# Kernel optimization log

Measured on AMD Instinct MI355X. Metric: run time of the kernel, lower is better.

The kernel has to match this reference:

```python
import jax, jax.numpy as jnp
import numpy as np

S = 128          # spatial grid size per axis
N = 100000       # active voxels
C_IN = 32
C_OUT = 32
FS = 3           # filter size per axis -> 27 offsets


def _build_rulebook():
    """Build submanifold-conv rulebook: for each active site and each of the
    27 filter offsets, the index of the active neighbor (or masked out)."""
    rng = np.random.default_rng(0)
    coords = rng.integers(0, S, size=(2 * N, 3))
    lin = coords[:, 0] * S * S + coords[:, 1] * S + coords[:, 2]
    lin = np.unique(lin)[:N]                      # sorted unique active sites
    xyz = np.stack([lin // (S * S), (lin // S) % S, lin % S], axis=1)  # [N,3]
    offs = np.stack(np.meshgrid(*([np.arange(FS) - FS // 2] * 3), indexing='ij'), -1).reshape(-1, 3)  # [27,3]
    nb = xyz[:, None, :] + offs[None, :, :]       # [N,27,3]
    inb = np.all((nb >= 0) & (nb < S), axis=-1)   # in-bounds
    nb_lin = nb[..., 0] * S * S + nb[..., 1] * S + nb[..., 2]
    pos = np.searchsorted(lin, nb_lin)
    pos_c = np.clip(pos, 0, N - 1)
    found = inb & (lin[pos_c] == nb_lin)
    nbr_idx = np.where(found, pos_c, 0).astype(np.int32)   # [N,27]
    return nbr_idx, found


def setup_inputs() -> dict:
    key = jax.random.key(0)
    k1, k2 = jax.random.split(key)
    nbr_idx, nbr_mask = _build_rulebook()
    K = FS ** 3
    std = (2.0 / C_IN / K) ** 0.5   # matches module init
    return {
        'features': jax.random.normal(k1, (N, C_IN), dtype=jnp.float32),
        'weight': std * jax.random.normal(k2, (K, C_IN, C_OUT), dtype=jnp.float32),
        'bias': jnp.zeros((C_OUT,), dtype=jnp.float32),
        'nbr_idx': jnp.asarray(nbr_idx),
        'nbr_mask': jnp.asarray(nbr_mask),
    }


def reference(features, weight, bias, nbr_idx, nbr_mask):
    # Submanifold sparse conv: gather active neighbors per filter offset,
    # multiply by per-offset [Cin,Cout] weight, accumulate at active sites.
    gathered = jnp.where(nbr_mask[:, :, None], features[nbr_idx], 0.0)  # [N,K,Cin]
    out = jnp.einsum('nki,kio->no', gathered, weight) + bias            # [N,Cout]
    return out
```

## Files before the change

### kernel.cpp

```cpp
#include <hip/hip_runtime.h>
#include <hip/hip_bf16.h>

#define NVOX 100000
#define CIN 32
#define COUT 32
#define KOFF 27
#define KPAD 28

typedef __attribute__((ext_vector_type(8))) short short8;
typedef __attribute__((ext_vector_type(4))) float float4v;
typedef __attribute__((ext_vector_type(4))) int   int4v;

__device__ __forceinline__ short f2bf(float x) {
    union { float f; unsigned u; } v; v.f = x;
    unsigned u = v.u;
    u += 0x7FFFu + ((u >> 16) & 1u);
    return (short)(u >> 16);
}

__global__ __launch_bounds__(256) void feat_cvt_kernel(
    const float* __restrict__ feat, unsigned short* __restrict__ fbf)
{
    int i = (blockIdx.x * 256 + threadIdx.x) * 4;
    if (i < NVOX * CIN) {
        float4v f = *(const float4v*)(feat + i);
        short s[4] = { f2bf(f.x), f2bf(f.y), f2bf(f.z), f2bf(f.w) };
        *(ulonglong1*)(fbf + i) = *(ulonglong1*)s;
    } else if (i < (NVOX + 1) * CIN) {
        short s[4] = { 0, 0, 0, 0 };
        *(ulonglong1*)(fbf + i) = *(ulonglong1*)s;
    }
}

__global__ __launch_bounds__(256) void wgt_cvt_kernel(
    const float* __restrict__ weight, short8* __restrict__ wfrag)
{
    int g = blockIdx.x * 256 + threadIdx.x;
    if (g >= KOFF * 2 * 64) return;
    int k   = g >> 7;
    int rem = g & 127;
    int t   = rem >> 6;
    int ln  = rem & 63;
    int co  = t * 16 + (ln & 15);
    int cib = (ln >> 4) * 8;
    const float* wp = weight + (k * CIN + cib) * COUT + co;
    short8 b;
#pragma unroll
    for (int j = 0; j < 8; ++j) b[j] = f2bf(wp[j * COUT]);
    wfrag[g] = b;
}

__global__ __launch_bounds__(256) void enc_fold_kernel(
    const int* __restrict__ nbr_idx, const int* __restrict__ nbr_mask,
    int* __restrict__ encb)
{
    int v = blockIdx.x * 4 + (threadIdx.x >> 6);
    int k = threadIdx.x & 63;
    if (v >= NVOX || k >= KPAD) return;
    int e;
    if (k < KOFF) {
        int id = nbr_idx[v * KOFF + k];
        int mk = nbr_mask[v * KOFF + k];
        e = (mk ? id : NVOX) << 6;
    } else {
        e = NVOX << 6;
    }
    encb[v * KPAD + k] = e;
}

__global__ __launch_bounds__(512, 4) void subm_conv_kernel(
    const unsigned short* __restrict__ fbf,
    const short8* __restrict__ wfrag,
    const float* __restrict__ bias,
    const int* __restrict__ encb,
    float* __restrict__ out)
{
    __shared__ short8 wlds[KOFF * 2 * 64];

    const int tid  = threadIdx.x;
    const int lane = tid & 63;
    const int wave = tid >> 6;
    const int m    = lane & 15;
    const int quad = lane >> 4;

    const int v0 = (blockIdx.x * 8 + wave) * 16;
    int v = v0 + m;
    if (v > NVOX - 1) v = NVOX - 1;

    const int4v* ep = (const int4v*)(encb + v * KPAD);
    int4v encv[7];
#pragma unroll
    for (int q = 0; q < 7; ++q) encv[q] = ep[q];
    const int* enc = (const int*)encv;

    for (int g = tid; g < KOFF * 2 * 64; g += 512) wlds[g] = wfrag[g];
    __syncthreads();

    float4v acc0 = {0.f, 0.f, 0.f, 0.f};
    float4v acc1 = {0.f, 0.f, 0.f, 0.f};

    const char* fb  = (const char*)fbf;
    const int   boff = quad * 16;

    short8 abuf[8];
#pragma unroll
    for (int k = 0; k < 8; ++k)
        abuf[k] = *(const short8*)(fb + (size_t)(unsigned)enc[k] + boff);

#pragma unroll
    for (int k = 0; k < KOFF; ++k) {
        const int slot = k & 7;
        short8 a = abuf[slot];
        if (k + 8 < KOFF)
            abuf[slot] = *(const short8*)(fb + (size_t)(unsigned)enc[k + 8] + boff);

        short8 wb0 = wlds[k * 128 + lane];
        short8 wb1 = wlds[k * 128 + 64 + lane];
        acc0 = __builtin_amdgcn_mfma_f32_16x16x32_bf16(a, wb0, acc0, 0, 0, 0);
        acc1 = __builtin_amdgcn_mfma_f32_16x16x32_bf16(a, wb1, acc1, 0, 0, 0);
    }

    const float bs0 = bias[m];
    const float bs1 = bias[16 + m];
#pragma unroll
    for (int r = 0; r < 4; ++r) {
        int vv = v0 + quad * 4 + r;
        if (vv < NVOX) {
            out[(size_t)vv * COUT + m]      = acc0[r] + bs0;
            out[(size_t)vv * COUT + 16 + m] = acc1[r] + bs1;
        }
    }
}

extern "C" void kernel_launch(void* const* d_in, const int* in_sizes, int n_in,
                              void* d_out, int out_size, void* d_ws, size_t ws_size,
                              hipStream_t stream) {
    const float* feat = (const float*)d_in[0];
    const float* wgt  = (const float*)d_in[1];
    const float* bias = (const float*)d_in[2];
    const int*   nidx = (const int*)d_in[3];
    const int*   nmsk = (const int*)d_in[4];
    float*       out  = (float*)d_out;

    unsigned short* fbf   = (unsigned short*)d_ws;
    short8*         wfrag = (short8*)((char*)d_ws + 6400064);
    int*            encb  = (int*)((char*)d_ws + 6400064 + 55296);

    feat_cvt_kernel<<<((NVOX + 1) * CIN / 4 + 255) / 256, 256, 0, stream>>>(feat, fbf);
    wgt_cvt_kernel<<<(KOFF * 2 * 64 + 255) / 256, 256, 0, stream>>>(wgt, wfrag);
    enc_fold_kernel<<<(NVOX + 3) / 4, 256, 0, stream>>>(nidx, nmsk, encb);

    const int block = 512;
    const int grid  = (NVOX + 127) / 128;
    subm_conv_kernel<<<grid, block, 0, stream>>>(fbf, wfrag, bias, encb, out);
}
```

Measured before the change: 115.7 us.

## Compact per-tile filter offsets to skip offsets with no active neighbors

Replaces the per-voxel encoded-neighbor table with a per-16-voxel-tile compaction kernel. It builds a ballot of the offsets where at least one voxel in the tile has a neighbor, and stores only those offsets' gather addresses and weight-slot indices. The conv kernel then loops over a dynamic count of live offsets, which should cut the gather loads, LDS weight reads and MFMAs spent on masked (zero) neighbors. In exchange the loop is no longer fully unrolled, the prefetch depth drops from 8 to about 2 in-flight gathers, and the preprocessing kernel is more expensive (LDS transpose plus serial per-offset writes).

```diff
diff --git a/kernel.cpp b/kernel.cpp
--- a/kernel.cpp
+++ b/kernel.cpp
@@ -5,11 +5,10 @@
 #define CIN 32
 #define COUT 32
 #define KOFF 27
-#define KPAD 28
+#define NTILE 6250
 
 typedef __attribute__((ext_vector_type(8))) short short8;
 typedef __attribute__((ext_vector_type(4))) float float4v;
-typedef __attribute__((ext_vector_type(4))) int   int4v;
 
 __device__ __forceinline__ short f2bf(float x) {
     union { float f; unsigned u; } v; v.f = x;
@@ -50,85 +49,123 @@
     wfrag[g] = b;
 }
 
-__global__ __launch_bounds__(256) void enc_fold_kernel(
+__global__ __launch_bounds__(256) void compact_kernel(
     const int* __restrict__ nbr_idx, const int* __restrict__ nbr_mask,
-    int* __restrict__ encb)
+    int* __restrict__ cenc, int* __restrict__ koff, int* __restrict__ cnt_g)
 {
-    int v = blockIdx.x * 4 + (threadIdx.x >> 6);
-    int k = threadIdx.x & 63;
-    if (v >= NVOX || k >= KPAD) return;
-    int e;
-    if (k < KOFF) {
-        int id = nbr_idx[v * KOFF + k];
-        int mk = nbr_mask[v * KOFF + k];
-        e = (mk ? id : NVOX) << 6;
-    } else {
-        e = NVOX << 6;
+    __shared__ int elds[4][KOFF * 17];
+    const int tid  = threadIdx.x;
+    const int lane = tid & 63;
+    const int wave = tid >> 6;
+    const int tile = blockIdx.x * 4 + wave;
+    if (tile >= NTILE) return;
+
+    const int base = tile * 16 * KOFF;
+#pragma unroll
+    for (int i = 0; i < 7; ++i) {
+        int p = lane + i * 64;
+        if (p < 16 * KOFF) {
+            int id = nbr_idx[base + p];
+            int mk = nbr_mask[base + p];
+            int v  = p / KOFF;
+            int k  = p - v * KOFF;
+            elds[wave][k * 17 + v] = (mk ? id : NVOX) << 6;
+        }
     }
-    encb[v * KPAD + k] = e;
+    int live = 0;
+    if (lane < KOFF) {
+#pragma unroll
+        for (int mm = 0; mm < 16; ++mm)
+            live |= (elds[wave][lane * 17 + mm] != (NVOX << 6));
+    }
+    unsigned long long bal = __ballot(live != 0);
+    int cnt = __popcll(bal);
+    int j = 0;
+    while (bal) {
+        int k = (int)__builtin_ctzll(bal);
+        bal &= bal - 1;
+        int e = elds[wave][k * 17 + (lane & 15)];
+        if (lane < 16) cenc[(tile * KOFF + j) * 16 + lane] = e;
+        if (lane == 0) koff[tile * 32 + j] = k * 128;
+        ++j;
+    }
+    if (cnt == 0) {
+        if (lane < 16) cenc[tile * KOFF * 16 + lane] = NVOX << 6;
+        if (lane == 0) koff[tile * 32] = 0;
+        cnt = 1;
+    }
+    if (lane == 0) cnt_g[tile] = cnt;
 }
 
 __global__ __launch_bounds__(512, 4) void subm_conv_kernel(
     const unsigned short* __restrict__ fbf,
     const short8* __restrict__ wfrag,
     const float* __restrict__ bias,
-    const int* __restrict__ encb,
+    const int* __restrict__ cenc,
+    const int* __restrict__ koff,
+    const int* __restrict__ cnt_g,
     float* __restrict__ out)
 {
     __shared__ short8 wlds[KOFF * 2 * 64];
 
-    const int tid  = threadIdx.x;
+    const int tid = threadIdx.x;
+    for (int g = tid; g < KOFF * 2 * 64; g += 512) wlds[g] = wfrag[g];
+
     const int lane = tid & 63;
     const int wave = tid >> 6;
     const int m    = lane & 15;
     const int quad = lane >> 4;
+    const int tile = blockIdx.x * 8 + wave;
 
-    const int v0 = (blockIdx.x * 8 + wave) * 16;
-    int v = v0 + m;
-    if (v > NVOX - 1) v = NVOX - 1;
+    __syncthreads();
+    if (tile >= NTILE) return;
 
-    const int4v* ep = (const int4v*)(encb + v * KPAD);
-    int4v encv[7];
-#pragma unroll
-    for (int q = 0; q < 7; ++q) encv[q] = ep[q];
-    const int* enc = (const int*)encv;
+    const int cnt = cnt_g[tile];
+    const int jm  = cnt - 1;
+    const int* cb = cenc + tile * KOFF * 16;
+    const int* kb = koff + tile * 32;
+    const char* fb = (const char*)fbf;
+    const int boff = quad * 16;
 
-    for (int g = tid; g < KOFF * 2 * 64; g += 512) wlds[g] = wfrag[g];
-    __syncthreads();
+    int j1 = 1 > jm ? jm : 1;
+    int j2 = 2 > jm ? jm : 2;
+    int ce0 = cb[m];
+    int ce1 = cb[j1 * 16 + m];
+    int ce2 = cb[j2 * 16 + m];
+    int ko0 = kb[0];
+    int ko1 = kb[j1];
+    short8 a0 = *(const short8*)(fb + (size_t)(unsigned)ce0 + boff);
+    short8 a1 = *(const short8*)(fb + (size_t)(unsigned)ce1 + boff);
 
     float4v acc0 = {0.f, 0.f, 0.f, 0.f};
     float4v acc1 = {0.f, 0.f, 0.f, 0.f};
 
-    const char* fb  = (const char*)fbf;
-    const int   boff = quad * 16;
+    for (int j = 0; j < cnt; ++j) {
+        short8 a = a0;
+        int   ko = ko0;
+        a0  = a1;
+        ko0 = ko1;
+        int ce_n = ce2;
+        int jn = j + 3; jn = jn > jm ? jm : jn;
+        ce2 = cb[jn * 16 + m];
+        int kn = j + 2; kn = kn > jm ? jm : kn;
+        ko1 = kb[kn];
+        a1 = *(const short8*)(fb + (size_t)(unsigned)ce_n + boff);
 
-    short8 abuf[8];
-#pragma unroll
-    for (int k = 0; k < 8; ++k)
-        abuf[k] = *(const short8*)(fb + (size_t)(unsigned)enc[k] + boff);
-
-#pragma unroll
-    for (int k = 0; k < KOFF; ++k) {
-        const int slot = k & 7;
-        short8 a = abuf[slot];
-        if (k + 8 < KOFF)
-            abuf[slot] = *(const short8*)(fb + (size_t)(unsigned)enc[k + 8] + boff);
-
-        short8 wb0 = wlds[k * 128 + lane];
-        short8 wb1 = wlds[k * 128 + 64 + lane];
+        short8 wb0 = wlds[ko + lane];
+        short8 wb1 = wlds[ko + 64 + lane];
         acc0 = __builtin_amdgcn_mfma_f32_16x16x32_bf16(a, wb0, acc0, 0, 0, 0);
         acc1 = __builtin_amdgcn_mfma_f32_16x16x32_bf16(a, wb1, acc1, 0, 0, 0);
     }
 
     const float bs0 = bias[m];
     const float bs1 = bias[16 + m];
+    const int v0 = tile * 16;
 #pragma unroll
     for (int r = 0; r < 4; ++r) {
         int vv = v0 + quad * 4 + r;
-        if (vv < NVOX) {
-            out[(size_t)vv * COUT + m]      = acc0[r] + bs0;
-            out[(size_t)vv * COUT + 16 + m] = acc1[r] + bs1;
-        }
+        out[(size_t)vv * COUT + m]      = acc0[r] + bs0;
+        out[(size_t)vv * COUT + 16 + m] = acc1[r] + bs1;
     }
 }
 
@@ -142,15 +179,18 @@
     const int*   nmsk = (const int*)d_in[4];
     float*       out  = (float*)d_out;
 
-    unsigned short* fbf   = (unsigned short*)d_ws;
-    short8*         wfrag = (short8*)((char*)d_ws + 6400064);
-    int*            encb  = (int*)((char*)d_ws + 6400064 + 55296);
+    char* ws = (char*)d_ws;
+    unsigned short* fbf   = (unsigned short*)ws;
+    short8*         wfrag = (short8*)(ws + 6400128);
+    int*            cenc  = (int*)(ws + 6455424);
+    int*            koff  = (int*)(ws + 17255424);
+    int*            cntg  = (int*)(ws + 18055424);
 
     feat_cvt_kernel<<<((NVOX + 1) * CIN / 4 + 255) / 256, 256, 0, stream>>>(feat, fbf);
     wgt_cvt_kernel<<<(KOFF * 2 * 64 + 255) / 256, 256, 0, stream>>>(wgt, wfrag);
-    enc_fold_kernel<<<(NVOX + 3) / 4, 256, 0, stream>>>(nidx, nmsk, encb);
+    compact_kernel<<<(NTILE + 3) / 4, 256, 0, stream>>>(nidx, nmsk, cenc, koff, cntg);
 
     const int block = 512;
-    const int grid  = (NVOX + 127) / 128;
-    subm_conv_kernel<<<grid, block, 0, stream>>>(fbf, wfrag, bias, encb, out);
+    const int grid  = (NTILE + 7) / 8;
+    subm_conv_kernel<<<grid, block, 0, stream>>>(fbf, wfrag, bias, cenc, koff, cntg, out);
 }
```

After: 128.9 us. +11.4%, slower.

## Fuse rulebook encoding into conv kernel via coalesced LDS staging

Applied to the files above, without the earlier changes.

Removes the separate enc_fold kernel and its padded encoded-index buffer. Each wave now loads its 16x27 neighbor indices and masks with coalesced int4 reads, encodes them into LDS, and reads per-row offsets from LDS in the gather loop. Block size drops from 512 to 256 threads with 4 tiles per block, which means more blocks each re-staging the 27x2x64 weight fragments into LDS. The goal is to save a kernel launch and a global round trip of roughly 11 MB, at the cost of more LDS use and more weight staging.

```diff
diff --git a/kernel.cpp b/kernel.cpp
--- a/kernel.cpp
+++ b/kernel.cpp
@@ -5,7 +5,7 @@
 #define CIN 32
 #define COUT 32
 #define KOFF 27
-#define KPAD 28
+#define NTILE 6250
 
 typedef __attribute__((ext_vector_type(8))) short short8;
 typedef __attribute__((ext_vector_type(4))) float float4v;
@@ -50,69 +50,76 @@
     wfrag[g] = b;
 }
 
-__global__ __launch_bounds__(256) void enc_fold_kernel(
-    const int* __restrict__ nbr_idx, const int* __restrict__ nbr_mask,
-    int* __restrict__ encb)
-{
-    int v = blockIdx.x * 4 + (threadIdx.x >> 6);
-    int k = threadIdx.x & 63;
-    if (v >= NVOX || k >= KPAD) return;
-    int e;
-    if (k < KOFF) {
-        int id = nbr_idx[v * KOFF + k];
-        int mk = nbr_mask[v * KOFF + k];
-        e = (mk ? id : NVOX) << 6;
-    } else {
-        e = NVOX << 6;
-    }
-    encb[v * KPAD + k] = e;
-}
-
-__global__ __launch_bounds__(512, 4) void subm_conv_kernel(
+__global__ __launch_bounds__(256, 4) void subm_conv_kernel(
     const unsigned short* __restrict__ fbf,
     const short8* __restrict__ wfrag,
     const float* __restrict__ bias,
-    const int* __restrict__ encb,
+    const int* __restrict__ nbr_idx,
+    const int* __restrict__ nbr_mask,
     float* __restrict__ out)
 {
     __shared__ short8 wlds[KOFF * 2 * 64];
+    __shared__ int    elds[4 * 16 * KOFF];
 
     const int tid  = threadIdx.x;
     const int lane = tid & 63;
     const int wave = tid >> 6;
     const int m    = lane & 15;
     const int quad = lane >> 4;
+    const int tile = blockIdx.x * 4 + wave;
+    const bool tv  = tile < NTILE;
 
-    const int v0 = (blockIdx.x * 8 + wave) * 16;
-    int v = v0 + m;
-    if (v > NVOX - 1) v = NVOX - 1;
+    const int base4 = tile * (16 * KOFF / 4);
+    int4v id0, id1, mk0, mk1;
+    const int p4a = lane, p4b = lane + 64;
+    if (tv) {
+        id0 = ((const int4v*)nbr_idx)[base4 + p4a];
+        mk0 = ((const int4v*)nbr_mask)[base4 + p4a];
+        if (p4b < 108) {
+            id1 = ((const int4v*)nbr_idx)[base4 + p4b];
+            mk1 = ((const int4v*)nbr_mask)[base4 + p4b];
+        }
+    }
 
-    const int4v* ep = (const int4v*)(encb + v * KPAD);
-    int4v encv[7];
-#pragma unroll
-    for (int q = 0; q < 7; ++q) encv[q] = ep[q];
-    const int* enc = (const int*)encv;
+    for (int g = tid; g < KOFF * 2 * 64; g += 256) wlds[g] = wfrag[g];
 
-    for (int g = tid; g < KOFF * 2 * 64; g += 512) wlds[g] = wfrag[g];
+    int* ew = elds + wave * (16 * KOFF);
+    if (tv) {
+        int4v e0, e1;
+        e0.x = mk0.x ? (id0.x << 6) : (NVOX << 6);
+        e0.y = mk0.y ? (id0.y << 6) : (NVOX << 6);
+        e0.z = mk0.z ? (id0.z << 6) : (NVOX << 6);
+        e0.w = mk0.w ? (id0.w << 6) : (NVOX << 6);
+        ((int4v*)ew)[p4a] = e0;
+        if (p4b < 108) {
+            e1.x = mk1.x ? (id1.x << 6) : (NVOX << 6);
+            e1.y = mk1.y ? (id1.y << 6) : (NVOX << 6);
+            e1.z = mk1.z ? (id1.z << 6) : (NVOX << 6);
+            e1.w = mk1.w ? (id1.w << 6) : (NVOX << 6);
+            ((int4v*)ew)[p4b] = e1;
+        }
+    }
     __syncthreads();
+    if (!tv) return;
+
+    const char* fb   = (const char*)fbf;
+    const int   boff = quad * 16;
+    const int*  em   = ew + m * KOFF;
 
     float4v acc0 = {0.f, 0.f, 0.f, 0.f};
     float4v acc1 = {0.f, 0.f, 0.f, 0.f};
 
-    const char* fb  = (const char*)fbf;
-    const int   boff = quad * 16;
-
     short8 abuf[8];
 #pragma unroll
     for (int k = 0; k < 8; ++k)
-        abuf[k] = *(const short8*)(fb + (size_t)(unsigned)enc[k] + boff);
+        abuf[k] = *(const short8*)(fb + (size_t)(unsigned)em[k] + boff);
 
 #pragma unroll
     for (int k = 0; k < KOFF; ++k) {
         const int slot = k & 7;
         short8 a = abuf[slot];
         if (k + 8 < KOFF)
-            abuf[slot] = *(const short8*)(fb + (size_t)(unsigned)enc[k + 8] + boff);
+            abuf[slot] = *(const short8*)(fb + (size_t)(unsigned)em[k + 8] + boff);
 
         short8 wb0 = wlds[k * 128 + lane];
         short8 wb1 = wlds[k * 128 + 64 + lane];
@@ -122,13 +129,12 @@
 
     const float bs0 = bias[m];
     const float bs1 = bias[16 + m];
+    const int v0 = tile * 16;
 #pragma unroll
     for (int r = 0; r < 4; ++r) {
         int vv = v0 + quad * 4 + r;
-        if (vv < NVOX) {
-            out[(size_t)vv * COUT + m]      = acc0[r] + bs0;
-            out[(size_t)vv * COUT + 16 + m] = acc1[r] + bs1;
-        }
+        out[(size_t)vv * COUT + m]      = acc0[r] + bs0;
+        out[(size_t)vv * COUT + 16 + m] = acc1[r] + bs1;
     }
 }
 
@@ -142,15 +148,14 @@
     const int*   nmsk = (const int*)d_in[4];
     float*       out  = (float*)d_out;
 
-    unsigned short* fbf   = (unsigned short*)d_ws;
-    short8*         wfrag = (short8*)((char*)d_ws + 6400064);
-    int*            encb  = (int*)((char*)d_ws + 6400064 + 55296);
+    char* ws = (char*)d_ws;
+    unsigned short* fbf   = (unsigned short*)ws;
+    short8*         wfrag = (short8*)(ws + 6400128);
 
     feat_cvt_kernel<<<((NVOX + 1) * CIN / 4 + 255) / 256, 256, 0, stream>>>(feat, fbf);
     wgt_cvt_kernel<<<(KOFF * 2 * 64 + 255) / 256, 256, 0, stream>>>(wgt, wfrag);
-    enc_fold_kernel<<<(NVOX + 3) / 4, 256, 0, stream>>>(nidx, nmsk, encb);
 
-    const int block = 512;
-    const int grid  = (NVOX + 127) / 128;
-    subm_conv_kernel<<<grid, block, 0, stream>>>(fbf, wfrag, bias, encb, out);
+    const int block = 256;
+    const int grid  = (NTILE + 3) / 4;
+    subm_conv_kernel<<<grid, block, 0, stream>>>(fbf, wfrag, bias, nidx, nmsk, out);
 }
```

Result: faster. 109.6 us (-5.3%).
